# Optimization experiments

Measured on AMD Instinct MI355X. Metric: run time of the kernel, lower is better.

## Reference

```python
import jax, jax.numpy as jnp
import numpy as np

N, E, D_IN, D_H, D_OUT = 50000, 600000, 128, 128, 1


def setup_inputs() -> dict:
    key = jax.random.key(0)
    ks = jax.random.split(key, 20)
    p = lambda k, sh: jax.random.normal(k, sh, dtype=jnp.float32) * 0.05
    return {
        "x": jax.random.normal(ks[0], (N, D_IN), dtype=jnp.float32),
        "edge_weight": jax.random.uniform(ks[1], (E,), dtype=jnp.float32),
        # input LEConv (lin1: W1/b1, lin2: W2 no bias, lin3: W3/b3)
        "W1_in": p(ks[2], (D_IN, D_H)), "b1_in": jnp.zeros((D_H,), jnp.float32),
        "W2_in": p(ks[3], (D_IN, D_H)),
        "W3_in": p(ks[4], (D_IN, D_H)), "b3_in": jnp.zeros((D_H,), jnp.float32),
        # inner LEConv
        "W1_h": p(ks[5], (D_H, D_H)), "b1_h": jnp.zeros((D_H,), jnp.float32),
        "W2_h": p(ks[6], (D_H, D_H)),
        "W3_h": p(ks[7], (D_H, D_H)), "b3_h": jnp.zeros((D_H,), jnp.float32),
        # output LEConv
        "W1_o": p(ks[8], (D_H, D_OUT)), "b1_o": jnp.zeros((D_OUT,), jnp.float32),
        "W2_o": p(ks[9], (D_H, D_OUT)),
        "W3_o": p(ks[10], (D_H, D_OUT)), "b3_o": jnp.zeros((D_OUT,), jnp.float32),
        # LayerNorms
        "g1": jnp.ones((D_H,), jnp.float32), "beta1": jnp.zeros((D_H,), jnp.float32),
        "g2": jnp.ones((D_H,), jnp.float32), "beta2": jnp.zeros((D_H,), jnp.float32),
        "edge_index": jax.random.randint(ks[11], (2, E), 0, N, dtype=jnp.int32),
        "number_of_layers": 4,
    }


def _leconv(x, src, dst, w, W1, b1, W2, W3, b3):
    # PyG LEConv: out_i = lin3(x_i) + sum_{j->i} w_e * (lin1(x_j) - lin2(x_i))
    a = x @ W1 + b1                                   # [N, D_out]
    b = x @ W2                                        # [N, D_out]
    wsum = jax.ops.segment_sum(w, dst, num_segments=N)             # [N]
    agg = jax.ops.segment_sum(w[:, None] * a[src], dst, num_segments=N)  # [N, D_out]
    return agg - b * wsum[:, None] + x @ W3 + b3


def _ln(x, g, b, eps=1e-5):
    m = x.mean(-1, keepdims=True)
    v = x.var(-1, keepdims=True)
    return (x - m) * jax.lax.rsqrt(v + eps) * g + b


def reference(x, edge_weight, W1_in, b1_in, W2_in, W3_in, b3_in,
              W1_h, b1_h, W2_h, W3_h, b3_h,
              W1_o, b1_o, W2_o, W3_o, b3_o,
              g1, beta1, g2, beta2, edge_index, number_of_layers):
    src, dst = edge_index[0], edge_index[1]
    # per-feature standardization over nodes (torch std is unbiased -> ddof=1)
    x = (x - x.mean(0, keepdims=True)) / (jnp.std(x, axis=0, ddof=1, keepdims=True) + 1e-6)
    h = jax.nn.leaky_relu(
        _ln(_leconv(x, src, dst, edge_weight, W1_in, b1_in, W2_in, W3_in, b3_in), g1, beta1),
        negative_slope=0.1)
    for _ in range(number_of_layers - 2):
        h = jax.nn.leaky_relu(
            _ln(_leconv(h, src, dst, edge_weight, W1_h, b1_h, W2_h, W3_h, b3_h), g2, beta2),
            negative_slope=0.1)
    h = _leconv(h, src, dst, edge_weight, W1_o, b1_o, W2_o, W3_o, b3_o)
    return jax.nn.sigmoid(h)
```

## Files before the change

### kernel.cpp

```cpp
#include <hip/hip_runtime.h>
#include <hip/hip_bf16.h>
#include <math.h>


typedef _Float16 f16x8 __attribute__((ext_vector_type(8)));
typedef _Float16 f16x4 __attribute__((ext_vector_type(4)));
typedef float f32x4 __attribute__((ext_vector_type(4)));

#define LSTRIDE 136

__device__ inline float wave_reduce_sum(float v) {
    #pragma unroll
    for (int off = 32; off > 0; off >>= 1)
        v += __shfl_xor(v, off, 64);
    return v;
}


__global__ __launch_bounds__(256) void hist_kernel(
    const int* __restrict__ dst, int* __restrict__ deg,
    int* __restrict__ rank, int E)
{
    int e = blockIdx.x * 256 + threadIdx.x;
    if (e < E) rank[e] = atomicAdd(&deg[dst[e]], 1);
}

__global__ __launch_bounds__(256) void scan_pass1(
    const int* __restrict__ deg, int N, int* __restrict__ partial)
{
    __shared__ int sh[256];
    int t = threadIdx.x;
    int base = blockIdx.x * 1024 + t * 4;
    int s = 0;
    #pragma unroll
    for (int i = 0; i < 4; ++i) { int idx = base + i; if (idx < N) s += deg[idx]; }
    sh[t] = s; __syncthreads();
    for (int off = 128; off > 0; off >>= 1) {
        if (t < off) sh[t] += sh[t + off];
        __syncthreads();
    }
    if (t == 0) partial[blockIdx.x] = sh[0];
}

__global__ __launch_bounds__(256) void scan_pass2(int* __restrict__ partial, int nb)
{
    __shared__ int sh[256];
    int t = threadIdx.x;
    sh[t] = (t < nb) ? partial[t] : 0;
    __syncthreads();
    for (int off = 1; off < 256; off <<= 1) {
        int x = sh[t];
        if (t >= off) x += sh[t - off];
        __syncthreads();
        sh[t] = x;
        __syncthreads();
    }
    if (t < nb) partial[t] = (t > 0) ? sh[t - 1] : 0;
}

__global__ __launch_bounds__(256) void scan_pass3(
    const int* __restrict__ deg, int N, const int* __restrict__ partial,
    int* __restrict__ rowptr, int E)
{
    __shared__ int sh[256];
    int t = threadIdx.x;
    int base = blockIdx.x * 1024 + t * 4;
    int v[4]; int s = 0;
    #pragma unroll
    for (int i = 0; i < 4; ++i) { int idx = base + i; v[i] = (idx < N) ? deg[idx] : 0; s += v[i]; }
    sh[t] = s; __syncthreads();
    for (int off = 1; off < 256; off <<= 1) {
        int x = sh[t];
        if (t >= off) x += sh[t - off];
        __syncthreads();
        sh[t] = x;
        __syncthreads();
    }
    int off0 = partial[blockIdx.x] + ((t > 0) ? sh[t - 1] : 0);
    #pragma unroll
    for (int i = 0; i < 4; ++i) {
        int idx = base + i;
        if (idx < N) { rowptr[idx] = off0; off0 += v[i]; }
    }
    if (blockIdx.x == 0 && t == 0) rowptr[N] = E;
}

__global__ __launch_bounds__(256) void csr_fill_kernel(
    const int* __restrict__ src, const int* __restrict__ dst,
    const float* __restrict__ ew, const int* __restrict__ rowptr,
    const int* __restrict__ rank, int2* __restrict__ csr, int E)
{
    int e = blockIdx.x * 256 + threadIdx.x;
    if (e >= E) return;
    int d = dst[e];
    int pos = rowptr[d] + rank[e];
    csr[pos] = make_int2(src[e], __float_as_int(ew[e]));
}

__global__ __launch_bounds__(256) void wsum_csr_kernel(
    const int* __restrict__ rowptr, const int2* __restrict__ csr,
    float* __restrict__ wsum, int N)
{
    int n = blockIdx.x * 256 + threadIdx.x;
    if (n >= N) return;
    int b = rowptr[n], en = rowptr[n + 1];
    float s = 0.f;
    for (int e = b; e < en; ++e) s += __int_as_float(csr[e].y);
    wsum[n] = s;
}


__global__ __launch_bounds__(256) void convert_weights_kernel(
    const float* __restrict__ W1a, const float* __restrict__ W2a,
    const float* __restrict__ W3a, _Float16* __restrict__ Wta,
    const float* __restrict__ W1b, const float* __restrict__ W2b,
    const float* __restrict__ W3b, _Float16* __restrict__ Wtb)
{
    int idx = blockIdx.x * 256 + threadIdx.x;
    if (idx >= 2 * 384 * 128) return;
    int set = idx >= 384 * 128;
    int id = idx - set * 384 * 128;
    int n = id >> 7, k = id & 127;
    const float* W = set ? ((n < 128) ? W1b : (n < 256) ? W2b : W3b)
                         : ((n < 128) ? W1a : (n < 256) ? W2a : W3a);
    _Float16* Wt = set ? Wtb : Wta;
    int c = n & 127;
    Wt[id] = (_Float16)W[k * 128 + c];
}


#define CS_BLOCKS 512

__global__ __launch_bounds__(256) void colstats_kernel(
    const float* __restrict__ x, int N,
    float* __restrict__ ps, float* __restrict__ pss)
{
    __shared__ float shs[256][4];
    __shared__ float shq[256][4];
    int t = threadIdx.x;
    int g = t >> 5;
    int c = t & 31;
    const float4* xv = (const float4*)x;
    const int S = CS_BLOCKS * 8;
    float s0=0.f,s1=0.f,s2=0.f,s3=0.f, q0=0.f,q1=0.f,q2=0.f,q3=0.f;
    int r = blockIdx.x * 8 + g;
    for (; r + 3*S < N; r += 4*S) {
        float4 v0 = xv[(size_t)r * 32 + c];
        float4 v1 = xv[(size_t)(r + S) * 32 + c];
        float4 v2 = xv[(size_t)(r + 2*S) * 32 + c];
        float4 v3 = xv[(size_t)(r + 3*S) * 32 + c];
        s0 += v0.x + v1.x + v2.x + v3.x;
        s1 += v0.y + v1.y + v2.y + v3.y;
        s2 += v0.z + v1.z + v2.z + v3.z;
        s3 += v0.w + v1.w + v2.w + v3.w;
        q0 += v0.x*v0.x + v1.x*v1.x + v2.x*v2.x + v3.x*v3.x;
        q1 += v0.y*v0.y + v1.y*v1.y + v2.y*v2.y + v3.y*v3.y;
        q2 += v0.z*v0.z + v1.z*v1.z + v2.z*v2.z + v3.z*v3.z;
        q3 += v0.w*v0.w + v1.w*v1.w + v2.w*v2.w + v3.w*v3.w;
    }
    for (; r < N; r += S) {
        float4 v = xv[(size_t)r * 32 + c];
        s0 += v.x; s1 += v.y; s2 += v.z; s3 += v.w;
        q0 += v.x*v.x; q1 += v.y*v.y; q2 += v.z*v.z; q3 += v.w*v.w;
    }
    shs[t][0]=s0; shs[t][1]=s1; shs[t][2]=s2; shs[t][3]=s3;
    shq[t][0]=q0; shq[t][1]=q1; shq[t][2]=q2; shq[t][3]=q3;
    __syncthreads();
    if (t < 32) {
        float S4[4] = {0,0,0,0}, Q4[4] = {0,0,0,0};
        #pragma unroll
        for (int gg = 0; gg < 8; ++gg) {
            #pragma unroll
            for (int i = 0; i < 4; ++i) {
                S4[i] += shs[t + 32*gg][i];
                Q4[i] += shq[t + 32*gg][i];
            }
        }
        #pragma unroll
        for (int i = 0; i < 4; ++i) {
            ps [blockIdx.x * 128 + t*4 + i] = S4[i];
            pss[blockIdx.x * 128 + t*4 + i] = Q4[i];
        }
    }
}

__global__ __launch_bounds__(256) void reduce_stats_kernel(
    const float* __restrict__ ps, const float* __restrict__ pss, int N,
    float* __restrict__ mean, float* __restrict__ rstd)
{
    __shared__ float sh[256];
    int t = threadIdx.x;
    int f = t & 127;
    const float* src = (t >= 128) ? pss : ps;
    float s = 0.f;
    int r = 0;
    for (; r + 4 <= CS_BLOCKS; r += 4) {
        float a0 = src[(r    ) * 128 + f];
        float a1 = src[(r + 1) * 128 + f];
        float a2 = src[(r + 2) * 128 + f];
        float a3 = src[(r + 3) * 128 + f];
        s += (a0 + a1) + (a2 + a3);
    }
    for (; r < CS_BLOCKS; ++r) s += src[r * 128 + f];
    sh[t] = s;
    __syncthreads();
    if (t < 128) {
        float sum = sh[t], sumsq = sh[t + 128];
        float m = sum / (float)N;
        float var = (sumsq - sum * sum / (float)N) / (float)(N - 1);
        var = fmaxf(var, 0.f);
        mean[t] = m;
        rstd[t] = 1.f / (sqrtf(var) + 1e-6f);
    }
}


__global__ __launch_bounds__(256, 2) void gemm_mfma_kernel(
    const _Float16* __restrict__ h, int N, int nTiles,
    const _Float16* __restrict__ Wt,
    const float* __restrict__ b1,
    const float* __restrict__ b3,
    const float* __restrict__ wsum,
    _Float16* __restrict__ out_a, _Float16* __restrict__ out_d)
{
    __shared__ _Float16 ldsS[64 * LSTRIDE];
    __shared__ _Float16 lds_a[64 * LSTRIDE];
    __shared__ _Float16 lds_d[64 * LSTRIDE];

    int t = threadIdx.x;
    int wave = t >> 6;
    int lane = t & 63;
    int quad = lane >> 4;
    int c16  = lane & 15;

    const f16x8* wv = (const f16x8*)Wt;
    int ntl[6] = {2*wave, 2*wave+1, 8+2*wave, 9+2*wave, 16+2*wave, 17+2*wave};
    f16x8 bfrag[6][4];
    #pragma unroll
    for (int j = 0; j < 6; ++j) {
        int nrow = ntl[j] * 16 + c16;
        #pragma unroll
        for (int s = 0; s < 4; ++s)
            bfrag[j][s] = wv[(size_t)nrow * 16 + s * 4 + quad];
    }
    float bb1[2], bb3[2];
    #pragma unroll
    for (int j = 0; j < 2; ++j) {
        int col = (2*wave + j) * 16 + c16;
        bb1[j] = b1[col];
        bb3[j] = b3[col];
    }

    const f16x8* hv = (const f16x8*)h;
    f16x8* oa = (f16x8*)out_a;
    f16x8* od = (f16x8*)out_d;

    for (int tile = blockIdx.x; tile < nTiles; tile += gridDim.x) {
        int row0 = tile * 64;

        #pragma unroll
        for (int i = 0; i < 4; ++i) {
            int idx = i * 256 + t;
            int row = idx >> 4;
            int chunk = idx & 15;
            int grow = row0 + row;
            if (grow >= N) grow = N - 1;
            *(f16x8*)&ldsS[row * LSTRIDE + chunk * 8] = hv[(size_t)grow * 16 + chunk];
        }
        __syncthreads();

        #pragma unroll
        for (int r = 0; r < 4; ++r) {
            f16x8 afrag[4];
            #pragma unroll
            for (int s = 0; s < 4; ++s)
                afrag[s] = *(const f16x8*)&ldsS[(r*16 + c16) * LSTRIDE + (s*4 + quad) * 8];

            f32x4 acc[6];
            #pragma unroll
            for (int j = 0; j < 6; ++j) acc[j] = (f32x4){0.f, 0.f, 0.f, 0.f};
            #pragma unroll
            for (int s = 0; s < 4; ++s) {
                #pragma unroll
                for (int j = 0; j < 6; ++j)
                    acc[j] = __builtin_amdgcn_mfma_f32_16x16x32_f16(afrag[s], bfrag[j][s], acc[j], 0, 0, 0);
            }

            float wsv[4];
            #pragma unroll
            for (int reg = 0; reg < 4; ++reg) {
                int gr = row0 + r*16 + quad*4 + reg;
                wsv[reg] = wsum[(gr < N) ? gr : (N - 1)];
            }
            #pragma unroll
            for (int j = 0; j < 2; ++j) {
                int col = (2*wave + j) * 16 + c16;
                #pragma unroll
                for (int reg = 0; reg < 4; ++reg) {
                    int lr = r*16 + quad*4 + reg;
                    lds_a[lr * LSTRIDE + col] = (_Float16)(acc[j][reg] + bb1[j]);
                    lds_d[lr * LSTRIDE + col] =
                        (_Float16)(acc[4+j][reg] + bb3[j] - wsv[reg] * acc[2+j][reg]);
                }
            }
        }
        __syncthreads();

        #pragma unroll
        for (int i = 0; i < 4; ++i) {
            int idx = i * 256 + t;
            int row = idx >> 4;
            int c8  = idx & 15;
            int grow = row0 + row;
            if (grow < N) {
                f16x8 va = *(const f16x8*)&lds_a[row * LSTRIDE + c8 * 8];
                oa[(size_t)grow * 16 + c8] = va;
                f16x8 vd = *(const f16x8*)&lds_d[row * LSTRIDE + c8 * 8];
                od[(size_t)grow * 16 + c8] = vd;
            }
        }
        __syncthreads();
    }
}


__global__ __launch_bounds__(256, 2) void gemm_mfma_std_kernel(
    const float* __restrict__ x,
    const float* __restrict__ meanp, const float* __restrict__ rstdp,
    int N, int nTiles,
    const _Float16* __restrict__ Wt,
    const float* __restrict__ b1,
    const float* __restrict__ b3,
    const float* __restrict__ wsum,
    _Float16* __restrict__ out_a, _Float16* __restrict__ out_d)
{
    __shared__ _Float16 ldsS[64 * LSTRIDE];
    __shared__ _Float16 lds_a[64 * LSTRIDE];
    __shared__ _Float16 lds_d[64 * LSTRIDE];

    int t = threadIdx.x;
    int wave = t >> 6;
    int lane = t & 63;
    int quad = lane >> 4;
    int c16  = lane & 15;

    const f16x8* wv = (const f16x8*)Wt;
    int ntl[6] = {2*wave, 2*wave+1, 8+2*wave, 9+2*wave, 16+2*wave, 17+2*wave};
    f16x8 bfrag[6][4];
    #pragma unroll
    for (int j = 0; j < 6; ++j) {
        int nrow = ntl[j] * 16 + c16;
        #pragma unroll
        for (int s = 0; s < 4; ++s)
            bfrag[j][s] = wv[(size_t)nrow * 16 + s * 4 + quad];
    }
    float bb1[2], bb3[2];
    #pragma unroll
    for (int j = 0; j < 2; ++j) {
        int col = (2*wave + j) * 16 + c16;
        bb1[j] = b1[col];
        bb3[j] = b3[col];
    }

    int c4 = t & 31;
    float4 mu = ((const float4*)meanp)[c4];
    float4 rs = ((const float4*)rstdp)[c4];

    const float4* xv = (const float4*)x;
    f16x8* oa = (f16x8*)out_a;
    f16x8* od = (f16x8*)out_d;

    for (int tile = blockIdx.x; tile < nTiles; tile += gridDim.x) {
        int row0 = tile * 64;

        #pragma unroll
        for (int i = 0; i < 8; ++i) {
            int idx = i * 256 + t;
            int row = idx >> 5;
            int grow = row0 + row;
            if (grow >= N) grow = N - 1;
            float4 v = xv[(size_t)grow * 32 + c4];
            f16x4 o;
            o.x = (_Float16)((v.x - mu.x) * rs.x);
            o.y = (_Float16)((v.y - mu.y) * rs.y);
            o.z = (_Float16)((v.z - mu.z) * rs.z);
            o.w = (_Float16)((v.w - mu.w) * rs.w);
            *(f16x4*)&ldsS[row * LSTRIDE + c4 * 4] = o;
        }
        __syncthreads();

        #pragma unroll
        for (int r = 0; r < 4; ++r) {
            f16x8 afrag[4];
            #pragma unroll
            for (int s = 0; s < 4; ++s)
                afrag[s] = *(const f16x8*)&ldsS[(r*16 + c16) * LSTRIDE + (s*4 + quad) * 8];

            f32x4 acc[6];
            #pragma unroll
            for (int j = 0; j < 6; ++j) acc[j] = (f32x4){0.f, 0.f, 0.f, 0.f};
            #pragma unroll
            for (int s = 0; s < 4; ++s) {
                #pragma unroll
                for (int j = 0; j < 6; ++j)
                    acc[j] = __builtin_amdgcn_mfma_f32_16x16x32_f16(afrag[s], bfrag[j][s], acc[j], 0, 0, 0);
            }

            float wsv[4];
            #pragma unroll
            for (int reg = 0; reg < 4; ++reg) {
                int gr = row0 + r*16 + quad*4 + reg;
                wsv[reg] = wsum[(gr < N) ? gr : (N - 1)];
            }
            #pragma unroll
            for (int j = 0; j < 2; ++j) {
                int col = (2*wave + j) * 16 + c16;
                #pragma unroll
                for (int reg = 0; reg < 4; ++reg) {
                    int lr = r*16 + quad*4 + reg;
                    lds_a[lr * LSTRIDE + col] = (_Float16)(acc[j][reg] + bb1[j]);
                    lds_d[lr * LSTRIDE + col] =
                        (_Float16)(acc[4+j][reg] + bb3[j] - wsv[reg] * acc[2+j][reg]);
                }
            }
        }
        __syncthreads();

        #pragma unroll
        for (int i = 0; i < 4; ++i) {
            int idx = i * 256 + t;
            int row = idx >> 4;
            int c8  = idx & 15;
            int grow = row0 + row;
            if (grow < N) {
                f16x8 va = *(const f16x8*)&lds_a[row * LSTRIDE + c8 * 8];
                oa[(size_t)grow * 16 + c8] = va;
                f16x8 vd = *(const f16x8*)&lds_d[row * LSTRIDE + c8 * 8];
                od[(size_t)grow * 16 + c8] = vd;
            }
        }
        __syncthreads();
    }
}


__global__ __launch_bounds__(256) void aggregate_ln_kernel(
    const int* __restrict__ rowptr, const int2* __restrict__ csr,
    const _Float16* __restrict__ a, const _Float16* __restrict__ d,
    const float* __restrict__ g, const float* __restrict__ beta,
    _Float16* __restrict__ out, int N)
{
    int wave = threadIdx.x >> 6;
    int lane = threadIdx.x & 63;
    int grp  = lane >> 4;
    int l    = lane & 15;
    int node = blockIdx.x * 4 + wave;
    if (node >= N) return;
    int b = rowptr[node], en = rowptr[node + 1];
    int deg = en - b;

    const f16x8* av = (const f16x8*)a;
    f16x8 dv = ((const f16x8*)d)[(size_t)node * 16 + l];
    float acc[8] = {0,0,0,0,0,0,0,0};

    int nk = (deg + 3) >> 2;
    int k = 0;
    for (; k + 4 <= nk; k += 4) {
        int2 p[4];
        #pragma unroll
        for (int j = 0; j < 4; ++j) {
            int idx = b + (k + j) * 4 + grp;
            int idc = (idx < en) ? idx : b;
            p[j] = csr[idc];
            if (idx >= en) p[j].y = 0;
        }
        f16x8 v[4];
        #pragma unroll
        for (int j = 0; j < 4; ++j)
            v[j] = av[(size_t)p[j].x * 16 + l];
        #pragma unroll
        for (int j = 0; j < 4; ++j) {
            float w = __int_as_float(p[j].y);
            #pragma unroll
            for (int i = 0; i < 8; ++i) acc[i] += w * (float)v[j][i];
        }
    }
    if (k < nk) {
        int2 p[4];
        #pragma unroll
        for (int j = 0; j < 4; ++j) {
            int idx = b + (k + j) * 4 + grp;
            int idc = (idx < en) ? idx : b;
            p[j] = csr[idc];
            if (idx >= en) p[j].y = 0;
        }
        f16x8 v[4];
        #pragma unroll
        for (int j = 0; j < 4; ++j)
            v[j] = av[(size_t)p[j].x * 16 + l];
        #pragma unroll
        for (int j = 0; j < 4; ++j) {
            float w = __int_as_float(p[j].y);
            #pragma unroll
            for (int i = 0; i < 8; ++i) acc[i] += w * (float)v[j][i];
        }
    }

    #pragma unroll
    for (int i = 0; i < 8; ++i) {
        acc[i] += __shfl_xor(acc[i], 16, 64);
        acc[i] += __shfl_xor(acc[i], 32, 64);
    }

    float v[8];
    float s = 0.f, ss = 0.f;
    #pragma unroll
    for (int i = 0; i < 8; ++i) {
        v[i] = acc[i] + (float)dv[i];
        s += v[i]; ss += v[i] * v[i];
    }
    #pragma unroll
    for (int off = 1; off <= 8; off <<= 1) {
        s  += __shfl_xor(s,  off, 64);
        ss += __shfl_xor(ss, off, 64);
    }
    float mean = s * (1.f / 128.f);
    float var = ss * (1.f / 128.f) - mean * mean;
    float rstd = rsqrtf(var + 1e-5f);

    const float4* gv4 = (const float4*)g;
    const float4* bv4 = (const float4*)beta;
    float4 ga = gv4[l*2], gb = gv4[l*2+1];
    float4 ba = bv4[l*2], bb = bv4[l*2+1];
    float go[8] = {ga.x,ga.y,ga.z,ga.w,gb.x,gb.y,gb.z,gb.w};
    float bo[8] = {ba.x,ba.y,ba.z,ba.w,bb.x,bb.y,bb.z,bb.w};
    f16x8 ov;
    #pragma unroll
    for (int i = 0; i < 8; ++i) {
        float o = (v[i] - mean) * rstd * go[i] + bo[i];
        o = o >= 0.f ? o : 0.1f * o;
        ov[i] = (_Float16)o;
    }
    if (grp == 0)
        ((f16x8*)out)[(size_t)node * 16 + l] = ov;
}


__global__ __launch_bounds__(256) void aggregate_out_kernel(
    const int* __restrict__ rowptr, const int2* __restrict__ csr,
    const _Float16* __restrict__ a, const _Float16* __restrict__ d,
    const float* __restrict__ g, const float* __restrict__ beta,
    const float* __restrict__ W1o, const float* __restrict__ b1o,
    const float* __restrict__ W2o,
    const float* __restrict__ W3o, const float* __restrict__ b3o,
    const float* __restrict__ wsum,
    float* __restrict__ a1, float* __restrict__ dpart, int N)
{
    int wave = threadIdx.x >> 6;
    int lane = threadIdx.x & 63;
    int grp  = lane >> 4;
    int l    = lane & 15;
    int node = blockIdx.x * 4 + wave;
    if (node >= N) return;
    int b = rowptr[node], en = rowptr[node + 1];
    int deg = en - b;

    const f16x8* av = (const f16x8*)a;
    f16x8 dv = ((const f16x8*)d)[(size_t)node * 16 + l];
    float wsn = wsum[node];
    float acc[8] = {0,0,0,0,0,0,0,0};

    int nk = (deg + 3) >> 2;
    int k = 0;
    for (; k + 4 <= nk; k += 4) {
        int2 p[4];
        #pragma unroll
        for (int j = 0; j < 4; ++j) {
            int idx = b + (k + j) * 4 + grp;
            int idc = (idx < en) ? idx : b;
            p[j] = csr[idc];
            if (idx >= en) p[j].y = 0;
        }
        f16x8 v[4];
        #pragma unroll
        for (int j = 0; j < 4; ++j)
            v[j] = av[(size_t)p[j].x * 16 + l];
        #pragma unroll
        for (int j = 0; j < 4; ++j) {
            float w = __int_as_float(p[j].y);
            #pragma unroll
            for (int i = 0; i < 8; ++i) acc[i] += w * (float)v[j][i];
        }
    }
    if (k < nk) {
        int2 p[4];
        #pragma unroll
        for (int j = 0; j < 4; ++j) {
            int idx = b + (k + j) * 4 + grp;
            int idc = (idx < en) ? idx : b;
            p[j] = csr[idc];
            if (idx >= en) p[j].y = 0;
        }
        f16x8 v[4];
        #pragma unroll
        for (int j = 0; j < 4; ++j)
            v[j] = av[(size_t)p[j].x * 16 + l];
        #pragma unroll
        for (int j = 0; j < 4; ++j) {
            float w = __int_as_float(p[j].y);
            #pragma unroll
            for (int i = 0; i < 8; ++i) acc[i] += w * (float)v[j][i];
        }
    }

    #pragma unroll
    for (int i = 0; i < 8; ++i) {
        acc[i] += __shfl_xor(acc[i], 16, 64);
        acc[i] += __shfl_xor(acc[i], 32, 64);
    }

    float v[8];
    float s = 0.f, ss = 0.f;
    #pragma unroll
    for (int i = 0; i < 8; ++i) {
        v[i] = acc[i] + (float)dv[i];
        s += v[i]; ss += v[i] * v[i];
    }
    #pragma unroll
    for (int off = 1; off <= 8; off <<= 1) {
        s  += __shfl_xor(s,  off, 64);
        ss += __shfl_xor(ss, off, 64);
    }
    float mean = s * (1.f / 128.f);
    float var = ss * (1.f / 128.f) - mean * mean;
    float rstd = rsqrtf(var + 1e-5f);

    const float4* gv4 = (const float4*)g;
    const float4* bv4 = (const float4*)beta;
    float4 ga = gv4[l*2], gb = gv4[l*2+1];
    float4 ba = bv4[l*2], bb = bv4[l*2+1];
    float go[8] = {ga.x,ga.y,ga.z,ga.w,gb.x,gb.y,gb.z,gb.w};
    float bo[8] = {ba.x,ba.y,ba.z,ba.w,bb.x,bb.y,bb.z,bb.w};

    float ho[8];
    #pragma unroll
    for (int i = 0; i < 8; ++i) {
        float o = (v[i] - mean) * rstd * go[i] + bo[i];
        o = o >= 0.f ? o : 0.1f * o;
        ho[i] = (float)(_Float16)o;
    }

    const float4* w1v = (const float4*)W1o;
    const float4* w2v = (const float4*)W2o;
    const float4* w3v = (const float4*)W3o;
    float4 w1a = w1v[l*2], w1b = w1v[l*2+1];
    float4 w2a = w2v[l*2], w2b = w2v[l*2+1];
    float4 w3a = w3v[l*2], w3b = w3v[l*2+1];
    float s1 = ho[0]*w1a.x + ho[1]*w1a.y + ho[2]*w1a.z + ho[3]*w1a.w
             + ho[4]*w1b.x + ho[5]*w1b.y + ho[6]*w1b.z + ho[7]*w1b.w;
    float s2 = ho[0]*w2a.x + ho[1]*w2a.y + ho[2]*w2a.z + ho[3]*w2a.w
             + ho[4]*w2b.x + ho[5]*w2b.y + ho[6]*w2b.z + ho[7]*w2b.w;
    float s3 = ho[0]*w3a.x + ho[1]*w3a.y + ho[2]*w3a.z + ho[3]*w3a.w
             + ho[4]*w3b.x + ho[5]*w3b.y + ho[6]*w3b.z + ho[7]*w3b.w;
    #pragma unroll
    for (int off = 1; off <= 8; off <<= 1) {
        s1 += __shfl_xor(s1, off, 64);
        s2 += __shfl_xor(s2, off, 64);
        s3 += __shfl_xor(s3, off, 64);
    }
    if (lane == 0) {
        a1[node] = s1 + b1o[0];
        dpart[node] = s3 + b3o[0] - wsn * s2;
    }
}


__global__ __launch_bounds__(256) void gather_out_kernel(
    const int* __restrict__ rowptr, const int2* __restrict__ csr,
    const float* __restrict__ a1, const float* __restrict__ dpart,
    float* __restrict__ out, int N)
{
    int n = blockIdx.x * 256 + threadIdx.x;
    if (n >= N) return;
    int b = rowptr[n], en = rowptr[n + 1];
    float s = dpart[n];
    int e = b;
    for (; e + 4 <= en; e += 4) {
        int2 p0 = csr[e], p1 = csr[e+1], p2 = csr[e+2], p3 = csr[e+3];
        float x0 = a1[p0.x], x1 = a1[p1.x], x2 = a1[p2.x], x3 = a1[p3.x];
        s += __int_as_float(p0.y) * x0 + __int_as_float(p1.y) * x1
           + __int_as_float(p2.y) * x2 + __int_as_float(p3.y) * x3;
    }
    for (; e < en; ++e) {
        int2 p = csr[e];
        s += __int_as_float(p.y) * a1[p.x];
    }
    out[n] = 1.f / (1.f + expf(-s));
}

extern "C" void kernel_launch(void* const* d_in, const int* in_sizes, int n_in,
                              void* d_out, int out_size, void* d_ws, size_t ws_size,
                              hipStream_t stream)
{
    const float* x     = (const float*)d_in[0];
    const float* ew    = (const float*)d_in[1];
    const float* W1_in = (const float*)d_in[2];
    const float* b1_in = (const float*)d_in[3];
    const float* W2_in = (const float*)d_in[4];
    const float* W3_in = (const float*)d_in[5];
    const float* b3_in = (const float*)d_in[6];
    const float* W1_h  = (const float*)d_in[7];
    const float* b1_h  = (const float*)d_in[8];
    const float* W2_h  = (const float*)d_in[9];
    const float* W3_h  = (const float*)d_in[10];
    const float* b3_h  = (const float*)d_in[11];
    const float* W1_o  = (const float*)d_in[12];
    const float* b1_o  = (const float*)d_in[13];
    const float* W2_o  = (const float*)d_in[14];
    const float* W3_o  = (const float*)d_in[15];
    const float* b3_o  = (const float*)d_in[16];
    const float* g1    = (const float*)d_in[17];
    const float* beta1 = (const float*)d_in[18];
    const float* g2    = (const float*)d_in[19];
    const float* beta2 = (const float*)d_in[20];
    const int*   eidx  = (const int*)d_in[21];

    const int N = in_sizes[0] / 128;
    const int E = in_sizes[1];
    const int* srcp = eidx;
    const int* dstp = eidx + E;

    size_t off = 0;
    auto carve = [&](size_t nbytes) -> void* {
        void* p = (char*)d_ws + off;
        off += (nbytes + 255) & ~(size_t)255;
        return p;
    };
    int*      deg    = (int*)     carve((size_t)N * 4);
    size_t zeroBytes = off;
    int*      rank   = (int*)     carve((size_t)E * 4);
    _Float16* buf_h  = (_Float16*)carve((size_t)N * 128 * 2);
    _Float16* buf_a  = (_Float16*)carve((size_t)N * 128 * 2);
    _Float16* buf_d  = (_Float16*)carve((size_t)N * 128 * 2);
    int2*     csr    = (int2*)    carve((size_t)E * 8);
    _Float16* Wt_in  = (_Float16*)carve(384 * 128 * 2);
    _Float16* Wt_h   = (_Float16*)carve(384 * 128 * 2);
    int*      rowptr = (int*)     carve((size_t)(N + 1) * 4);
    int*      partial= (int*)     carve(256 * 4);
    float*    ps     = (float*)   carve((size_t)CS_BLOCKS * 128 * 4);
    float*    pss    = (float*)   carve((size_t)CS_BLOCKS * 128 * 4);
    float*    meanp  = (float*)   carve(128 * 4);
    float*    rstdp  = (float*)   carve(128 * 4);
    float*    wsum   = (float*)   carve((size_t)N * 4);
    float*    a1     = (float*)   carve((size_t)N * 4);
    float*    dpart  = (float*)   carve((size_t)N * 4);

    const int nodeWaveBlocks = (N + 3) / 4;
    const int eBlocks = (E + 255) / 256;
    const int nBlocks = (N + 255) / 256;
    const int nb = (N + 1023) / 1024;
    const int wBlocks = (2 * 384 * 128 + 255) / 256;

    hipMemsetAsync(deg, 0, zeroBytes, stream);

    hist_kernel<<<eBlocks, 256, 0, stream>>>(dstp, deg, rank, E);
    scan_pass1<<<nb, 256, 0, stream>>>(deg, N, partial);
    scan_pass2<<<1, 256, 0, stream>>>(partial, nb);
    scan_pass3<<<nb, 256, 0, stream>>>(deg, N, partial, rowptr, E);
    csr_fill_kernel<<<eBlocks, 256, 0, stream>>>(srcp, dstp, ew, rowptr, rank, csr, E);
    wsum_csr_kernel<<<nBlocks, 256, 0, stream>>>(rowptr, csr, wsum, N);
    convert_weights_kernel<<<wBlocks, 256, 0, stream>>>(
        W1_in, W2_in, W3_in, Wt_in, W1_h, W2_h, W3_h, Wt_h);

    colstats_kernel<<<CS_BLOCKS, 256, 0, stream>>>(x, N, ps, pss);
    reduce_stats_kernel<<<1, 256, 0, stream>>>(ps, pss, N, meanp, rstdp);

    const int nTiles = (N + 63) / 64;
    const int gemmGrid = (nTiles < 512) ? nTiles : 512;

    gemm_mfma_std_kernel<<<gemmGrid, 256, 0, stream>>>(
        x, meanp, rstdp, N, nTiles, Wt_in, b1_in, b3_in, wsum, buf_a, buf_d);
    aggregate_ln_kernel<<<nodeWaveBlocks, 256, 0, stream>>>(rowptr, csr, buf_a, buf_d, g1, beta1, buf_h, N);

    gemm_mfma_kernel<<<gemmGrid, 256, 0, stream>>>(buf_h, N, nTiles, Wt_h, b1_h, b3_h, wsum, buf_a, buf_d);
    aggregate_ln_kernel<<<nodeWaveBlocks, 256, 0, stream>>>(rowptr, csr, buf_a, buf_d, g2, beta2, buf_h, N);

    gemm_mfma_kernel<<<gemmGrid, 256, 0, stream>>>(buf_h, N, nTiles, Wt_h, b1_h, b3_h, wsum, buf_a, buf_d);
    aggregate_out_kernel<<<nodeWaveBlocks, 256, 0, stream>>>(
        rowptr, csr, buf_a, buf_d, g2, beta2,
        W1_o, b1_o, W2_o, W3_o, b3_o, wsum, a1, dpart, N);

    gather_out_kernel<<<nBlocks, 256, 0, stream>>>(rowptr, csr, a1, dpart, (float*)d_out, N);
}
```

Baseline: 326.2 us.

## Merge preprocessing kernels to cut launch count and fuse wsum into histogram

The separate colstats, weight conversion and memset launches are merged into one prep kernel with block-range dispatch, which also zeroes deg/wsum. wsum is now accumulated with float atomics during the histogram pass instead of a separate CSR pass. Scan passes 1 and 2 merge through a last-block-done counter. The final stats reduction becomes 128 extra blocks of the CSR fill kernel. The aim is to remove several small launches and their serialization. In exchange it adds float atomics, which make wsum order-nondeterministic, and the single-wave scan only holds for up to 64 scan blocks.

```diff
diff --git a/kernel.cpp b/kernel.cpp
--- a/kernel.cpp
+++ b/kernel.cpp
@@ -8,27 +8,109 @@
 typedef float f32x4 __attribute__((ext_vector_type(4)));
 
 #define LSTRIDE 136
-
-__device__ inline float wave_reduce_sum(float v) {
-    #pragma unroll
-    for (int off = 32; off > 0; off >>= 1)
-        v += __shfl_xor(v, off, 64);
-    return v;
-}
-
-
-__global__ __launch_bounds__(256) void hist_kernel(
-    const int* __restrict__ dst, int* __restrict__ deg,
-    int* __restrict__ rank, int E)
+#define CS_BLOCKS 512
+
+
+__global__ __launch_bounds__(256) void prep_kernel(
+    const float* __restrict__ x, int N,
+    float* __restrict__ ps, float* __restrict__ pss,
+    const float* __restrict__ W1a, const float* __restrict__ W2a,
+    const float* __restrict__ W3a, _Float16* __restrict__ Wta,
+    const float* __restrict__ W1b, const float* __restrict__ W2b,
+    const float* __restrict__ W3b, _Float16* __restrict__ Wtb,
+    int* __restrict__ deg, float* __restrict__ wsum, int* __restrict__ counter)
+{
+    __shared__ float shs[256][4];
+    __shared__ float shq[256][4];
+    int bid = blockIdx.x;
+    int t = threadIdx.x;
+
+    if (bid < CS_BLOCKS) {
+        int g = t >> 5;
+        int c = t & 31;
+        const float4* xv = (const float4*)x;
+        const int S = CS_BLOCKS * 8;
+        float s0=0.f,s1=0.f,s2=0.f,s3=0.f, q0=0.f,q1=0.f,q2=0.f,q3=0.f;
+        int r = bid * 8 + g;
+        for (; r + 3*S < N; r += 4*S) {
+            float4 v0 = xv[(size_t)r * 32 + c];
+            float4 v1 = xv[(size_t)(r + S) * 32 + c];
+            float4 v2 = xv[(size_t)(r + 2*S) * 32 + c];
+            float4 v3 = xv[(size_t)(r + 3*S) * 32 + c];
+            s0 += v0.x + v1.x + v2.x + v3.x;
+            s1 += v0.y + v1.y + v2.y + v3.y;
+            s2 += v0.z + v1.z + v2.z + v3.z;
+            s3 += v0.w + v1.w + v2.w + v3.w;
+            q0 += v0.x*v0.x + v1.x*v1.x + v2.x*v2.x + v3.x*v3.x;
+            q1 += v0.y*v0.y + v1.y*v1.y + v2.y*v2.y + v3.y*v3.y;
+            q2 += v0.z*v0.z + v1.z*v1.z + v2.z*v2.z + v3.z*v3.z;
+            q3 += v0.w*v0.w + v1.w*v1.w + v2.w*v2.w + v3.w*v3.w;
+        }
+        for (; r < N; r += S) {
+            float4 v = xv[(size_t)r * 32 + c];
+            s0 += v.x; s1 += v.y; s2 += v.z; s3 += v.w;
+            q0 += v.x*v.x; q1 += v.y*v.y; q2 += v.z*v.z; q3 += v.w*v.w;
+        }
+        shs[t][0]=s0; shs[t][1]=s1; shs[t][2]=s2; shs[t][3]=s3;
+        shq[t][0]=q0; shq[t][1]=q1; shq[t][2]=q2; shq[t][3]=q3;
+        __syncthreads();
+        if (t < 32) {
+            float S4[4] = {0,0,0,0}, Q4[4] = {0,0,0,0};
+            #pragma unroll
+            for (int gg = 0; gg < 8; ++gg) {
+                #pragma unroll
+                for (int i = 0; i < 4; ++i) {
+                    S4[i] += shs[t + 32*gg][i];
+                    Q4[i] += shq[t + 32*gg][i];
+                }
+            }
+            #pragma unroll
+            for (int i = 0; i < 4; ++i) {
+                ps [bid * 128 + t*4 + i] = S4[i];
+                pss[bid * 128 + t*4 + i] = Q4[i];
+            }
+        }
+        return;
+    }
+
+    if (bid < CS_BLOCKS + 384) {
+        int idx = (bid - CS_BLOCKS) * 256 + t;
+        int set = idx >= 384 * 128;
+        int id = idx - set * 384 * 128;
+        int n = id >> 7, k = id & 127;
+        const float* W = set ? ((n < 128) ? W1b : (n < 256) ? W2b : W3b)
+                             : ((n < 128) ? W1a : (n < 256) ? W2a : W3a);
+        _Float16* Wt = set ? Wtb : Wta;
+        int c = n & 127;
+        Wt[id] = (_Float16)W[k * 128 + c];
+        return;
+    }
+
+    int idx = (bid - CS_BLOCKS - 384) * 256 + t;
+    for (int i = idx; i < N; i += 128 * 256) { deg[i] = 0; wsum[i] = 0.f; }
+    if (idx == 0) *counter = 0;
+}
+
+
+__global__ __launch_bounds__(256) void hist_wsum_kernel(
+    const int* __restrict__ dst, const float* __restrict__ ew,
+    int* __restrict__ deg, int* __restrict__ rank,
+    float* __restrict__ wsum, int E)
 {
     int e = blockIdx.x * 256 + threadIdx.x;
-    if (e < E) rank[e] = atomicAdd(&deg[dst[e]], 1);
-}
-
-__global__ __launch_bounds__(256) void scan_pass1(
-    const int* __restrict__ deg, int N, int* __restrict__ partial)
+    if (e < E) {
+        int d = dst[e];
+        rank[e] = atomicAdd(&deg[d], 1);
+        atomicAdd(&wsum[d], ew[e]);
+    }
+}
+
+__global__ __launch_bounds__(256) void scanA_kernel(
+    const int* __restrict__ deg, int N, int* __restrict__ partial,
+    int* __restrict__ counter)
 {
     __shared__ int sh[256];
+    __shared__ int lastFlag;
     int t = threadIdx.x;
     int base = blockIdx.x * 1024 + t * 4;
     int s = 0;
@@ -39,23 +121,25 @@
         if (t < off) sh[t] += sh[t + off];
         __syncthreads();
     }
-    if (t == 0) partial[blockIdx.x] = sh[0];
-}
-
-__global__ __launch_bounds__(256) void scan_pass2(int* __restrict__ partial, int nb)
-{
-    __shared__ int sh[256];
-    int t = threadIdx.x;
-    sh[t] = (t < nb) ? partial[t] : 0;
+    if (t == 0) {
+        atomicExch(&partial[blockIdx.x], sh[0]);
+        __threadfence();
+        int tk = atomicAdd(counter, 1);
+        lastFlag = (tk == (int)gridDim.x - 1) ? 1 : 0;
+    }
     __syncthreads();
-    for (int off = 1; off < 256; off <<= 1) {
-        int x = sh[t];
-        if (t >= off) x += sh[t - off];
-        __syncthreads();
-        sh[t] = x;
-        __syncthreads();
-    }
-    if (t < nb) partial[t] = (t > 0) ? sh[t - 1] : 0;
+    if (lastFlag && t < 64) {
+        __threadfence();
+        int nb = (int)gridDim.x;
+        int o = (t < nb) ? atomicAdd(&partial[t], 0) : 0;
+        int v = o;
+        #pragma unroll
+        for (int off = 1; off < 64; off <<= 1) {
+            int u = __shfl_up(v, off, 64);
+            if (t >= off) v += u;
+        }
+        if (t < nb) atomicExch(&partial[t], v - o);
+    }
 }
 
 __global__ __launch_bounds__(256) void scan_pass3(
@@ -85,132 +169,40 @@
     if (blockIdx.x == 0 && t == 0) rowptr[N] = E;
 }
 
-__global__ __launch_bounds__(256) void csr_fill_kernel(
+__global__ __launch_bounds__(256) void csr_fill_stats_kernel(
     const int* __restrict__ src, const int* __restrict__ dst,
     const float* __restrict__ ew, const int* __restrict__ rowptr,
-    const int* __restrict__ rank, int2* __restrict__ csr, int E)
-{
-    int e = blockIdx.x * 256 + threadIdx.x;
-    if (e >= E) return;
-    int d = dst[e];
-    int pos = rowptr[d] + rank[e];
-    csr[pos] = make_int2(src[e], __float_as_int(ew[e]));
-}
-
-__global__ __launch_bounds__(256) void wsum_csr_kernel(
-    const int* __restrict__ rowptr, const int2* __restrict__ csr,
-    float* __restrict__ wsum, int N)
-{
-    int n = blockIdx.x * 256 + threadIdx.x;
-    if (n >= N) return;
-    int b = rowptr[n], en = rowptr[n + 1];
-    float s = 0.f;
-    for (int e = b; e < en; ++e) s += __int_as_float(csr[e].y);
-    wsum[n] = s;
-}
-
-
-__global__ __launch_bounds__(256) void convert_weights_kernel(
-    const float* __restrict__ W1a, const float* __restrict__ W2a,
-    const float* __restrict__ W3a, _Float16* __restrict__ Wta,
-    const float* __restrict__ W1b, const float* __restrict__ W2b,
-    const float* __restrict__ W3b, _Float16* __restrict__ Wtb)
-{
-    int idx = blockIdx.x * 256 + threadIdx.x;
-    if (idx >= 2 * 384 * 128) return;
-    int set = idx >= 384 * 128;
-    int id = idx - set * 384 * 128;
-    int n = id >> 7, k = id & 127;
-    const float* W = set ? ((n < 128) ? W1b : (n < 256) ? W2b : W3b)
-                         : ((n < 128) ? W1a : (n < 256) ? W2a : W3a);
-    _Float16* Wt = set ? Wtb : Wta;
-    int c = n & 127;
-    Wt[id] = (_Float16)W[k * 128 + c];
-}
-
-
-#define CS_BLOCKS 512
-
-__global__ __launch_bounds__(256) void colstats_kernel(
-    const float* __restrict__ x, int N,
-    float* __restrict__ ps, float* __restrict__ pss)
-{
-    __shared__ float shs[256][4];
-    __shared__ float shq[256][4];
+    const int* __restrict__ rank, int2* __restrict__ csr, int E, int eBlocks,
+    const float* __restrict__ ps, const float* __restrict__ pss, int Nn,
+    float* __restrict__ mean, float* __restrict__ rstd)
+{
+    int bid = blockIdx.x;
     int t = threadIdx.x;
-    int g = t >> 5;
-    int c = t & 31;
-    const float4* xv = (const float4*)x;
-    const int S = CS_BLOCKS * 8;
-    float s0=0.f,s1=0.f,s2=0.f,s3=0.f, q0=0.f,q1=0.f,q2=0.f,q3=0.f;
-    int r = blockIdx.x * 8 + g;
-    for (; r + 3*S < N; r += 4*S) {
-        float4 v0 = xv[(size_t)r * 32 + c];
-        float4 v1 = xv[(size_t)(r + S) * 32 + c];
-        float4 v2 = xv[(size_t)(r + 2*S) * 32 + c];
-        float4 v3 = xv[(size_t)(r + 3*S) * 32 + c];
-        s0 += v0.x + v1.x + v2.x + v3.x;
-        s1 += v0.y + v1.y + v2.y + v3.y;
-        s2 += v0.z + v1.z + v2.z + v3.z;
-        s3 += v0.w + v1.w + v2.w + v3.w;
-        q0 += v0.x*v0.x + v1.x*v1.x + v2.x*v2.x + v3.x*v3.x;
-        q1 += v0.y*v0.y + v1.y*v1.y + v2.y*v2.y + v3.y*v3.y;
-        q2 += v0.z*v0.z + v1.z*v1.z + v2.z*v2.z + v3.z*v3.z;
-        q3 += v0.w*v0.w + v1.w*v1.w + v2.w*v2.w + v3.w*v3.w;
-    }
-    for (; r < N; r += S) {
-        float4 v = xv[(size_t)r * 32 + c];
-        s0 += v.x; s1 += v.y; s2 += v.z; s3 += v.w;
-        q0 += v.x*v.x; q1 += v.y*v.y; q2 += v.z*v.z; q3 += v.w*v.w;
-    }
-    shs[t][0]=s0; shs[t][1]=s1; shs[t][2]=s2; shs[t][3]=s3;
-    shq[t][0]=q0; shq[t][1]=q1; shq[t][2]=q2; shq[t][3]=q3;
-    __syncthreads();
-    if (t < 32) {
-        float S4[4] = {0,0,0,0}, Q4[4] = {0,0,0,0};
-        #pragma unroll
-        for (int gg = 0; gg < 8; ++gg) {
-            #pragma unroll
-            for (int i = 0; i < 4; ++i) {
-                S4[i] += shs[t + 32*gg][i];
-                Q4[i] += shq[t + 32*gg][i];
-            }
-        }
-        #pragma unroll
-        for (int i = 0; i < 4; ++i) {
-            ps [blockIdx.x * 128 + t*4 + i] = S4[i];
-            pss[blockIdx.x * 128 + t*4 + i] = Q4[i];
-        }
-    }
-}
-
-__global__ __launch_bounds__(256) void reduce_stats_kernel(
-    const float* __restrict__ ps, const float* __restrict__ pss, int N,
-    float* __restrict__ mean, float* __restrict__ rstd)
-{
-    __shared__ float sh[256];
-    int t = threadIdx.x;
-    int f = t & 127;
-    const float* src = (t >= 128) ? pss : ps;
-    float s = 0.f;
-    int r = 0;
-    for (; r + 4 <= CS_BLOCKS; r += 4) {
-        float a0 = src[(r    ) * 128 + f];
-        float a1 = src[(r + 1) * 128 + f];
-        float a2 = src[(r + 2) * 128 + f];
-        float a3 = src[(r + 3) * 128 + f];
-        s += (a0 + a1) + (a2 + a3);
-    }
-    for (; r < CS_BLOCKS; ++r) s += src[r * 128 + f];
-    sh[t] = s;
-    __syncthreads();
-    if (t < 128) {
-        float sum = sh[t], sumsq = sh[t + 128];
-        float m = sum / (float)N;
-        float var = (sumsq - sum * sum / (float)N) / (float)(N - 1);
+    if (bid < eBlocks) {
+        int e = bid * 256 + t;
+        if (e >= E) return;
+        int d = dst[e];
+        int pos = rowptr[d] + rank[e];
+        csr[pos] = make_int2(src[e], __float_as_int(ew[e]));
+        return;
+    }
+    __shared__ float sh1[256], sh2[256];
+    int f = bid - eBlocks;
+    int r0 = t * 2;
+    float s1 = ps [(size_t)r0 * 128 + f] + ps [(size_t)(r0 + 1) * 128 + f];
+    float s2 = pss[(size_t)r0 * 128 + f] + pss[(size_t)(r0 + 1) * 128 + f];
+    sh1[t] = s1; sh2[t] = s2; __syncthreads();
+    for (int off = 128; off > 0; off >>= 1) {
+        if (t < off) { sh1[t] += sh1[t + off]; sh2[t] += sh2[t + off]; }
+        __syncthreads();
+    }
+    if (t == 0) {
+        float sum = sh1[0], sumsq = sh2[0];
+        float m = sum / (float)Nn;
+        float var = (sumsq - sum * sum / (float)Nn) / (float)(Nn - 1);
         var = fmaxf(var, 0.f);
-        mean[t] = m;
-        rstd[t] = 1.f / (sqrtf(var) + 1e-6f);
+        mean[f] = m;
+        rstd[f] = 1.f / (sqrtf(var) + 1e-6f);
     }
 }
 
@@ -737,7 +729,6 @@
         return p;
     };
     int*      deg    = (int*)     carve((size_t)N * 4);
-    size_t zeroBytes = off;
     int*      rank   = (int*)     carve((size_t)E * 4);
     _Float16* buf_h  = (_Float16*)carve((size_t)N * 128 * 2);
     _Float16* buf_a  = (_Float16*)carve((size_t)N * 128 * 2);
@@ -747,6 +738,7 @@
     _Float16* Wt_h   = (_Float16*)carve(384 * 128 * 2);
     int*      rowptr = (int*)     carve((size_t)(N + 1) * 4);
     int*      partial= (int*)     carve(256 * 4);
+    int*      counter= (int*)     carve(256 * 4);
     float*    ps     = (float*)   carve((size_t)CS_BLOCKS * 128 * 4);
     float*    pss    = (float*)   carve((size_t)CS_BLOCKS * 128 * 4);
     float*    meanp  = (float*)   carve(128 * 4);
@@ -759,21 +751,20 @@
     const int eBlocks = (E + 255) / 256;
     const int nBlocks = (N + 255) / 256;
     const int nb = (N + 1023) / 1024;
-    const int wBlocks = (2 * 384 * 128 + 255) / 256;
-
-    hipMemsetAsync(deg, 0, zeroBytes, stream);
-
-    hist_kernel<<<eBlocks, 256, 0, stream>>>(dstp, deg, rank, E);
-    scan_pass1<<<nb, 256, 0, stream>>>(deg, N, partial);
-    scan_pass2<<<1, 256, 0, stream>>>(partial, nb);
+
+    prep_kernel<<<CS_BLOCKS + 384 + 128, 256, 0, stream>>>(
+        x, N, ps, pss,
+        W1_in, W2_in, W3_in, Wt_in, W1_h, W2_h, W3_h, Wt_h,
+        deg, wsum, counter);
+
+    hist_wsum_kernel<<<eBlocks, 256, 0, stream>>>(dstp, ew, deg, rank, wsum, E);
+
+    scanA_kernel<<<nb, 256, 0, stream>>>(deg, N, partial, counter);
     scan_pass3<<<nb, 256, 0, stream>>>(deg, N, partial, rowptr, E);
-    csr_fill_kernel<<<eBlocks, 256, 0, stream>>>(srcp, dstp, ew, rowptr, rank, csr, E);
-    wsum_csr_kernel<<<nBlocks, 256, 0, stream>>>(rowptr, csr, wsum, N);
-    convert_weights_kernel<<<wBlocks, 256, 0, stream>>>(
-        W1_in, W2_in, W3_in, Wt_in, W1_h, W2_h, W3_h, Wt_h);
-
-    colstats_kernel<<<CS_BLOCKS, 256, 0, stream>>>(x, N, ps, pss);
-    reduce_stats_kernel<<<1, 256, 0, stream>>>(ps, pss, N, meanp, rstdp);
+
+    csr_fill_stats_kernel<<<eBlocks + 128, 256, 0, stream>>>(
+        srcp, dstp, ew, rowptr, rank, csr, E, eBlocks,
+        ps, pss, N, meanp, rstdp);
 
     const int nTiles = (N + 63) / 64;
     const int gemmGrid = (nTiles < 512) ? nTiles : 512;
```

Measured after the change: 338.7 us. +3.8%, slower.
